# Performance work log

Measured on AMD Instinct MI355X. Metric: run time of the kernel, lower is better.

Reference implementation:

```python
import jax, jax.numpy as jnp
import numpy as np

MAX_SCALE_MUL = float(np.log(100.0))
EPS = 1e-12

def _l2norm(t):
    # F.normalize(dim=-1): x / max(||x||_2, eps)
    n = jnp.sqrt(jnp.sum(t * t, axis=-1, keepdims=True))
    return t / jnp.maximum(n, EPS)

def setup_inputs() -> dict:
    key = jax.random.key(0)
    ks = jax.random.split(key, 6)
    B, L, C, H = 2, 2048, 1024, 16
    x = jax.random.normal(ks[0], (B, L, C), dtype=jnp.float32)
    attn_bias = jax.random.normal(ks[1], (1, 1, L, L), dtype=jnp.float32) * 0.02
    W_qkv = jax.random.normal(ks[2], (3 * C, C), dtype=jnp.float32) * (1.0 / np.sqrt(C))
    q_bias = jnp.zeros((C,), dtype=jnp.float32)
    v_bias = jnp.zeros((C,), dtype=jnp.float32)
    scale_mul_1H11 = jnp.full((1, H, 1, 1), np.log(4.0), dtype=jnp.float32)
    W_proj = jax.random.normal(ks[3], (C, C), dtype=jnp.float32) * (1.0 / np.sqrt(C))
    b_proj = jnp.zeros((C,), dtype=jnp.float32)
    return {"x": x, "attn_bias": attn_bias, "W_qkv": W_qkv, "q_bias": q_bias,
            "v_bias": v_bias, "scale_mul_1H11": scale_mul_1H11,
            "W_proj": W_proj, "b_proj": b_proj}

def reference(x, attn_bias, W_qkv, q_bias, v_bias, scale_mul_1H11, W_proj, b_proj):
    B, L, C = x.shape
    H = scale_mul_1H11.shape[1]
    D = C // H
    # qkv projection (no linear bias) + concatenated (q_bias, 0, v_bias)
    bias = jnp.concatenate([q_bias, jnp.zeros_like(q_bias), v_bias])
    pre_qkv = jnp.einsum('blc,oc->blo', x, W_qkv) + bias  # (B,L,3C)
    qkv = pre_qkv.reshape(B, L, 3, H, D).transpose(2, 0, 3, 1, 4)  # (3,B,H,L,D)
    q, k, v = qkv[0], qkv[1], qkv[2]
    # cosine attention: l2-normalize q,k; q scaled by learned per-head scale
    scale_mul = jnp.exp(jnp.minimum(scale_mul_1H11, MAX_SCALE_MUL))
    q = _l2norm(q) * scale_mul
    k = _l2norm(k)
    # slow_attn_original with scale=1 (attn_l2_norm path)
    attn = jnp.einsum('bhld,bhmd->bhlm', q, k) + attn_bias  # (B,H,L,L)
    attn = jax.nn.softmax(attn, axis=-1)
    oup = jnp.einsum('bhlm,bhmd->bhld', attn, v)  # (B,H,L,D)
    oup = oup.transpose(0, 2, 1, 3).reshape(B, L, C)
    return jnp.einsum('blc,oc->blo', oup, W_proj) + b_proj
```

## Files before the change

### kernel.cpp

```cpp
#include <hip/hip_runtime.h>

typedef short bf16x8 __attribute__((ext_vector_type(8)));
typedef unsigned short u16x8 __attribute__((ext_vector_type(8)));
typedef float f32x4 __attribute__((ext_vector_type(4)));
typedef float f32x16 __attribute__((ext_vector_type(16)));
typedef unsigned int u32x2 __attribute__((ext_vector_type(2)));

#define LOG2E 1.44269504088896340736f

__device__ __forceinline__ float bf2f(unsigned short u) {
  union { unsigned int i; float f; } v; v.i = ((unsigned int)u) << 16; return v.f;
}
__device__ __forceinline__ unsigned short f2bf(float f) {
  union { float fl; unsigned int i; } v; v.fl = f;
  unsigned int r = v.i + 0x7FFFu + ((v.i >> 16) & 1u);
  return (unsigned short)(r >> 16);
}
__device__ __forceinline__ unsigned int cvt_pk_bf16(float lo, float hi) {
  unsigned int d;
  asm("v_cvt_pk_bf16_f32 %0, %1, %2" : "=v"(d) : "v"(lo), "v"(hi));
  return d;
}
__device__ __forceinline__ void perm_swap(unsigned int& a, unsigned int& b) {
  asm("v_permlane32_swap_b32 %0, %1" : "+v"(a), "+v"(b));
}
__device__ __forceinline__ bf16x8 mk8(unsigned int a, unsigned int b,
                                      unsigned int c, unsigned int d) {
  union { unsigned int u[4]; bf16x8 v; } r;
  r.u[0] = a; r.u[1] = b; r.u[2] = c; r.u[3] = d;
  return r.v;
}
__device__ __forceinline__ void gload_lds16(const void* g, void* l) {
  __builtin_amdgcn_global_load_lds(
      (const __attribute__((address_space(1))) void*)g,
      (__attribute__((address_space(3))) void*)l, 16, 0, 0);
}

__global__ __launch_bounds__(256) void cvt_all(const float* __restrict__ x,
                                               const float* __restrict__ wqkv,
                                               const float* __restrict__ wproj,
                                               unsigned short* __restrict__ xb,
                                               unsigned short* __restrict__ wqb,
                                               unsigned short* __restrict__ wpb) {
  int i = blockIdx.x * 256 + threadIdx.x;
  const float* src; unsigned short* dst; int off;
  if (i < 524288)       { src = x;     dst = xb;  off = i; }
  else if (i < 917504)  { src = wqkv;  dst = wqb; off = i - 524288; }
  else                  { src = wproj; dst = wpb; off = i - 917504; }
  float4 a = ((const float4*)src)[2 * off];
  float4 b = ((const float4*)src)[2 * off + 1];
  u16x8 o;
  o[0] = f2bf(a.x); o[1] = f2bf(a.y); o[2] = f2bf(a.z); o[3] = f2bf(a.w);
  o[4] = f2bf(b.x); o[5] = f2bf(b.y); o[6] = f2bf(b.z); o[7] = f2bf(b.w);
  ((u16x8*)dst)[off] = o;
}

__global__ __launch_bounds__(256) void prep_bias(const float* __restrict__ bias,
                                                 unsigned short* __restrict__ biasArr) {
  int tid = blockIdx.x * 256 + threadIdx.x;
  int kg = tid & 1;
  int l = (tid >> 1) & 63;
  int w = (tid >> 7) & 3;
  int kb = (tid >> 9) & 31;
  int qt = (tid >> 14) & 15;
  int q = qt * 128 + w * 32 + (l & 31);
  int kbase = kb * 64 + kg * 32 + (l >> 5) * 4;
  const float* src = bias + (size_t)q * 2048 + kbase;
  u16x8 oa, ob;
#pragma unroll
  for (int rr = 0; rr < 4; ++rr) {
    float4 g = *(const float4*)(src + rr * 8);
    unsigned short e0 = f2bf(g.x * LOG2E), e1 = f2bf(g.y * LOG2E);
    unsigned short e2 = f2bf(g.z * LOG2E), e3 = f2bf(g.w * LOG2E);
    if (rr < 2) {
      oa[rr * 4 + 0] = e0; oa[rr * 4 + 1] = e1; oa[rr * 4 + 2] = e2; oa[rr * 4 + 3] = e3;
    } else {
      ob[(rr - 2) * 4 + 0] = e0; ob[(rr - 2) * 4 + 1] = e1;
      ob[(rr - 2) * 4 + 2] = e2; ob[(rr - 2) * 4 + 3] = e3;
    }
  }
  int base = (((qt * 32 + kb) * 4 + w) * 4 + kg * 2) * 64 + l;
  ((u16x8*)biasArr)[base] = oa;
  ((u16x8*)biasArr)[base + 64] = ob;
}

template <bool F32OUT>
__global__ __launch_bounds__(256) void gemm_nt(const unsigned short* __restrict__ A,
                                               const unsigned short* __restrict__ B,
                                               void* __restrict__ Cout,
                                               const float* __restrict__ bias,
                                               int M, int N, int K) {
  __shared__ __align__(16) unsigned short a_lds[128 * 64];
  __shared__ __align__(16) unsigned short b_lds[128 * 64];
  const int t = threadIdx.x;
  const int lane = t & 63, w = t >> 6;
  const int wm = w >> 1, wn = w & 1;
  const int r16 = lane >> 4, c16 = lane & 15;
  const int m0 = blockIdx.y * 128, n0 = blockIdx.x * 128;
  f32x4 acc[4][4] = {};
  for (int k0 = 0; k0 < K; k0 += 64) {
#pragma unroll
    for (int i = 0; i < 4; ++i) {
      int s = i * 256 + t;
      int row = s >> 3, c = s & 7;
      int cs = c ^ (row & 7);
      gload_lds16(A + (size_t)(m0 + row) * K + k0 + cs * 8, (char*)a_lds + s * 16);
      gload_lds16(B + (size_t)(n0 + row) * K + k0 + cs * 8, (char*)b_lds + s * 16);
    }
    __syncthreads();
#pragma unroll
    for (int ks = 0; ks < 2; ++ks) {
      bf16x8 af[4], bfr[4];
#pragma unroll
      for (int mi = 0; mi < 4; ++mi) {
        int row = wm * 64 + mi * 16 + c16;
        int ch = (r16 + ks * 4) ^ (row & 7);
        af[mi] = *(const bf16x8*)&a_lds[row * 64 + ch * 8];
      }
#pragma unroll
      for (int ni = 0; ni < 4; ++ni) {
        int row = wn * 64 + ni * 16 + c16;
        int ch = (r16 + ks * 4) ^ (row & 7);
        bfr[ni] = *(const bf16x8*)&b_lds[row * 64 + ch * 8];
      }
#pragma unroll
      for (int mi = 0; mi < 4; ++mi)
#pragma unroll
        for (int ni = 0; ni < 4; ++ni)
          acc[mi][ni] = __builtin_amdgcn_mfma_f32_16x16x32_bf16(af[mi], bfr[ni], acc[mi][ni], 0, 0, 0);
    }
    __syncthreads();
  }
#pragma unroll
  for (int mi = 0; mi < 4; ++mi)
#pragma unroll
    for (int ni = 0; ni < 4; ++ni)
#pragma unroll
      for (int r = 0; r < 4; ++r) {
        int m = m0 + wm * 64 + mi * 16 + r16 * 4 + r;
        int n = n0 + wn * 64 + ni * 16 + c16;
        float v = acc[mi][ni][r];
        if constexpr (F32OUT) {
          ((float*)Cout)[(size_t)m * N + n] = v + bias[n];
        } else {
          ((unsigned short*)Cout)[(size_t)m * N + n] = f2bf(v);
        }
      }
}

template <bool F32OUT>
__global__ __launch_bounds__(256) void gemm_nt64(const unsigned short* __restrict__ A,
                                                 const unsigned short* __restrict__ B,
                                                 void* __restrict__ Cout,
                                                 const float* __restrict__ bias,
                                                 int M, int N, int K) {
  __shared__ __align__(16) unsigned short a_lds[128 * 64];
  __shared__ __align__(16) unsigned short b_lds[64 * 64];
  const int t = threadIdx.x;
  const int lane = t & 63, w = t >> 6;
  const int wm = w >> 1, wn = w & 1;
  const int r16 = lane >> 4, c16 = lane & 15;
  const int m0 = blockIdx.y * 128, n0 = blockIdx.x * 64;
  f32x4 acc[4][2] = {};
  for (int k0 = 0; k0 < K; k0 += 64) {
#pragma unroll
    for (int i = 0; i < 4; ++i) {
      int s = i * 256 + t;
      int row = s >> 3, c = s & 7;
      int cs = c ^ (row & 7);
      gload_lds16(A + (size_t)(m0 + row) * K + k0 + cs * 8, (char*)a_lds + s * 16);
    }
#pragma unroll
    for (int i = 0; i < 2; ++i) {
      int s = i * 256 + t;
      int row = s >> 3, c = s & 7;
      int cs = c ^ (row & 7);
      gload_lds16(B + (size_t)(n0 + row) * K + k0 + cs * 8, (char*)b_lds + s * 16);
    }
    __syncthreads();
#pragma unroll
    for (int ks = 0; ks < 2; ++ks) {
      bf16x8 af[4], bfr[2];
#pragma unroll
      for (int mi = 0; mi < 4; ++mi) {
        int row = wm * 64 + mi * 16 + c16;
        int ch = (r16 + ks * 4) ^ (row & 7);
        af[mi] = *(const bf16x8*)&a_lds[row * 64 + ch * 8];
      }
#pragma unroll
      for (int ni = 0; ni < 2; ++ni) {
        int row = wn * 32 + ni * 16 + c16;
        int ch = (r16 + ks * 4) ^ (row & 7);
        bfr[ni] = *(const bf16x8*)&b_lds[row * 64 + ch * 8];
      }
#pragma unroll
      for (int mi = 0; mi < 4; ++mi)
#pragma unroll
        for (int ni = 0; ni < 2; ++ni)
          acc[mi][ni] = __builtin_amdgcn_mfma_f32_16x16x32_bf16(af[mi], bfr[ni], acc[mi][ni], 0, 0, 0);
    }
    __syncthreads();
  }
#pragma unroll
  for (int mi = 0; mi < 4; ++mi)
#pragma unroll
    for (int ni = 0; ni < 2; ++ni)
#pragma unroll
      for (int r = 0; r < 4; ++r) {
        int m = m0 + wm * 64 + mi * 16 + r16 * 4 + r;
        int n = n0 + wn * 32 + ni * 16 + c16;
        float v = acc[mi][ni][r];
        if constexpr (F32OUT) {
          ((float*)Cout)[(size_t)m * N + n] = v + bias[n];
        } else {
          ((unsigned short*)Cout)[(size_t)m * N + n] = f2bf(v);
        }
      }
}

__global__ __launch_bounds__(256) void norm_pack(const unsigned short* __restrict__ pre,
                                                 const float* __restrict__ q_bias,
                                                 const float* __restrict__ v_bias,
                                                 const float* __restrict__ scale_mul,
                                                 unsigned short* __restrict__ qo,
                                                 unsigned short* __restrict__ ko,
                                                 unsigned short* __restrict__ vto) {
  __shared__ float tl[64][65];
  const int t = threadIdx.x;
  const int li = t >> 2, dq = t & 3;
  const int tile = blockIdx.x;
  const int sl = blockIdx.y;
  const int qkv = sl >> 4, h = sl & 15;
  const int b = tile >> 5, lt = tile & 31;
  const int l = lt * 64 + li;
  const int dbase = dq * 16;
  const unsigned short* src = pre + ((size_t)b * 2048 + l) * 3072 + qkv * 1024 + h * 64 + dbase;
  float v[16];
  bf16x8 x0 = *(const bf16x8*)src;
  bf16x8 x1 = *(const bf16x8*)(src + 8);
#pragma unroll
  for (int j = 0; j < 8; ++j) {
    v[j] = bf2f((unsigned short)x0[j]);
    v[8 + j] = bf2f((unsigned short)x1[j]);
  }
  if (qkv == 0) {
#pragma unroll
    for (int j = 0; j < 16; ++j) v[j] += q_bias[h * 64 + dbase + j];
  } else if (qkv == 2) {
#pragma unroll
    for (int j = 0; j < 16; ++j) v[j] += v_bias[h * 64 + dbase + j];
  }
  if (qkv < 2) {
    float ss = 0.f;
#pragma unroll
    for (int j = 0; j < 16; ++j) ss += v[j] * v[j];
    ss += __shfl_xor(ss, 1);
    ss += __shfl_xor(ss, 2);
    float inv = 1.0f / fmaxf(sqrtf(ss), 1e-12f);
    if (qkv == 0) inv *= __expf(fminf(scale_mul[h], 4.6051701859880914f));
    u16x8 o0, o1;
#pragma unroll
    for (int j = 0; j < 8; ++j) {
      o0[j] = f2bf(v[j] * inv);
      o1[j] = f2bf(v[8 + j] * inv);
    }
    unsigned short* dst = (qkv == 0 ? qo : ko) + ((size_t)(b * 16 + h) * 2048 + l) * 64 + dbase;
    *(u16x8*)dst = o0;
    *(u16x8*)(dst + 8) = o1;
  } else {
#pragma unroll
    for (int j = 0; j < 16; ++j) tl[li][dbase + j] = v[j];
    __syncthreads();
    const int d = li;
    const int lb = dq * 16;
    u16x8 o0, o1;
#pragma unroll
    for (int j = 0; j < 8; ++j) {
      o0[j] = f2bf(tl[lb + j][d]);
      o1[j] = f2bf(tl[lb + 8 + j][d]);
    }
    unsigned short* dst = vto + ((size_t)(b * 16 + h) * 64 + d) * 2048 + lt * 64 + lb;
    *(u16x8*)dst = o0;
    *(u16x8*)(dst + 8) = o1;
  }
}

__global__ __launch_bounds__(512, 4) void attn_fwd(const unsigned short* __restrict__ qb,
                                                   const unsigned short* __restrict__ kbuf,
                                                   const unsigned short* __restrict__ vtb,
                                                   const unsigned short* __restrict__ biasArr,
                                                   unsigned short* __restrict__ oup) {
  __shared__ __align__(16) unsigned short k_lds[2][4096];
  __shared__ __align__(16) unsigned short vt_lds[2][4096];
  __shared__ __align__(16) unsigned short b_lds[2][8192];
  const int t = threadIdx.x;
  const int lane = t & 63, w = t >> 6;
  const int sp = w >> 2;
  const int wq = w & 3;
  const int tt = t & 255;
  const int l31 = lane & 31, hi = lane >> 5;
  const int bid = blockIdx.x;
  const int swz = (bid & 7) * 64 + (bid >> 3);
  const int bh = swz >> 4;
  const int qt = swz & 15;
  const int q0 = qt * 128;
  const int h = bh & 15;
  const size_t base = (size_t)bh * 2048 * 64;
  const unsigned short* kp = kbuf + base + (size_t)(tt & 31) * 64 +
                             ((tt >> 6) & 3) * 16 + ((tt >> 5) & 1) * 8;
  const unsigned short* vp = vtb + base + (size_t)(tt & 31) * 2048 +
                             ((tt >> 6) & 3) * 16 + ((tt >> 5) & 1) * 8;
  const unsigned short* bsrc = biasArr + (size_t)qt * 262144 + tt * 8;
  bf16x8 qf[4];
  {
    const unsigned short* qp = qb + base + (size_t)(q0 + wq * 32 + l31) * 64 + hi * 8;
    qf[0] = *(const bf16x8*)qp;
    qf[1] = *(const bf16x8*)(qp + 16);
    qf[2] = *(const bf16x8*)(qp + 32);
    qf[3] = *(const bf16x8*)(qp + 48);
  }
  f32x16 o0 = {}, o1 = {};
  float ls = 0.f;

  for (int kbl = 0; kbl < 16; ++kbl) {
    const int kb = sp * 16 + kbl;
    gload_lds16(kp + (size_t)kb * 4096, (char*)k_lds[sp] + tt * 16);
    gload_lds16(kp + (size_t)kb * 4096 + 2048, (char*)k_lds[sp] + tt * 16 + 4096);
    gload_lds16(vp + kb * 64, (char*)vt_lds[sp] + tt * 16);
    gload_lds16(vp + kb * 64 + 32 * 2048, (char*)vt_lds[sp] + tt * 16 + 4096);
#pragma unroll
    for (int i = 0; i < 4; ++i)
      gload_lds16(bsrc + kb * 8192 + i * 2048, (char*)b_lds[sp] + tt * 16 + i * 4096);
    __syncthreads();
    const unsigned short* bl = b_lds[sp] + wq * 2048 + lane * 8;
#pragma unroll
    for (int kg = 0; kg < 2; ++kg) {
      f32x16 s = {};
      __builtin_amdgcn_s_setprio(1);
#pragma unroll
      for (int dc = 0; dc < 4; ++dc) {
        bf16x8 kf = *(const bf16x8*)&k_lds[sp][(kg * 4 + dc) * 512 + lane * 8];
        s = __builtin_amdgcn_mfma_f32_32x32x16_bf16(kf, qf[dc], s, 0, 0, 0);
      }
      __builtin_amdgcn_s_setprio(0);
      bf16x8 b0 = *(const bf16x8*)(bl + kg * 1024);
      bf16x8 b1 = *(const bf16x8*)(bl + kg * 1024 + 512);
      float p[16];
#pragma unroll
      for (int r = 0; r < 8; ++r) {
        p[r] = __builtin_amdgcn_exp2f(__builtin_fmaf(s[r], LOG2E, bf2f((unsigned short)b0[r])));
        p[8 + r] = __builtin_amdgcn_exp2f(__builtin_fmaf(s[8 + r], LOG2E, bf2f((unsigned short)b1[r])));
      }
#pragma unroll
      for (int r = 0; r < 16; ++r) ls += p[r];
      unsigned int x0 = cvt_pk_bf16(p[0], p[1]), x1 = cvt_pk_bf16(p[2], p[3]);
      unsigned int y0 = cvt_pk_bf16(p[4], p[5]), y1 = cvt_pk_bf16(p[6], p[7]);
      unsigned int z0 = cvt_pk_bf16(p[8], p[9]), z1 = cvt_pk_bf16(p[10], p[11]);
      unsigned int w0 = cvt_pk_bf16(p[12], p[13]), w1 = cvt_pk_bf16(p[14], p[15]);
      perm_swap(x0, y0); perm_swap(x1, y1); perm_swap(z0, w0); perm_swap(z1, w1);
      bf16x8 pfa = mk8(x0, x1, y0, y1);
      bf16x8 pfb = mk8(z0, z1, w0, w1);
      __builtin_amdgcn_s_setprio(1);
#pragma unroll
      for (int kc = 0; kc < 2; ++kc) {
        bf16x8 pfx = kc ? pfb : pfa;
        bf16x8 vf0 = *(const bf16x8*)&vt_lds[sp][(kg * 2 + kc) * 512 + lane * 8];
        bf16x8 vf1 = *(const bf16x8*)&vt_lds[sp][(4 + kg * 2 + kc) * 512 + lane * 8];
        o0 = __builtin_amdgcn_mfma_f32_32x32x16_bf16(vf0, pfx, o0, 0, 0, 0);
        o1 = __builtin_amdgcn_mfma_f32_32x32x16_bf16(vf1, pfx, o1, 0, 0, 0);
      }
      __builtin_amdgcn_s_setprio(0);
    }
    __syncthreads();
  }
  float* fO = (float*)b_lds;
  float* fL = (float*)k_lds;
  const int slot = wq * 64 + lane;
  if (sp == 1) {
#pragma unroll
    for (int i = 0; i < 16; ++i) {
      fO[i * 256 + slot] = o0[i];
      fO[(16 + i) * 256 + slot] = o1[i];
    }
    fL[slot] = ls;
  }
  __syncthreads();
  if (sp == 0) {
#pragma unroll
    for (int i = 0; i < 16; ++i) {
      o0[i] += fO[i * 256 + slot];
      o1[i] += fO[(16 + i) * 256 + slot];
    }
    ls += fL[slot];
    float lsum = ls + __shfl_xor(ls, 32);
    float inv = 1.0f / lsum;
    const int b = bh >> 4;
    unsigned short* orow = oup + ((size_t)b * 2048 + q0 + wq * 32 + l31) * 1024 + h * 64;
#pragma unroll
    for (int dg = 0; dg < 2; ++dg) {
#pragma unroll
      for (int rr = 0; rr < 4; ++rr) {
        float v0 = (dg ? o1[rr * 4 + 0] : o0[rr * 4 + 0]) * inv;
        float v1 = (dg ? o1[rr * 4 + 1] : o0[rr * 4 + 1]) * inv;
        float v2 = (dg ? o1[rr * 4 + 2] : o0[rr * 4 + 2]) * inv;
        float v3 = (dg ? o1[rr * 4 + 3] : o0[rr * 4 + 3]) * inv;
        u32x2 pk2;
        pk2[0] = cvt_pk_bf16(v0, v1);
        pk2[1] = cvt_pk_bf16(v2, v3);
        int d = dg * 32 + rr * 8 + hi * 4;
        *(u32x2*)(orow + d) = pk2;
      }
    }
  }
}

extern "C" void kernel_launch(void* const* d_in, const int* in_sizes, int n_in,
                              void* d_out, int out_size, void* d_ws, size_t ws_size,
                              hipStream_t stream) {
  const float* x = (const float*)d_in[0];
  const float* attn_bias = (const float*)d_in[1];
  const float* W_qkv = (const float*)d_in[2];
  const float* q_bias = (const float*)d_in[3];
  const float* v_bias = (const float*)d_in[4];
  const float* scale_mul = (const float*)d_in[5];
  const float* W_proj = (const float*)d_in[6];
  const float* b_proj = (const float*)d_in[7];
  float* out = (float*)d_out;
  char* ws = (char*)d_ws;

  unsigned short* x_bf = (unsigned short*)(ws + 0);
  unsigned short* wqkv_bf = (unsigned short*)(ws + 8388608);
  unsigned short* wproj_bf = (unsigned short*)(ws + 14680064);
  unsigned short* biasArr = (unsigned short*)(ws + 16777216);
  unsigned short* q_pk = (unsigned short*)(ws + 25165824);
  unsigned short* k_pk = (unsigned short*)(ws + 33554432);
  unsigned short* vt_pk = (unsigned short*)(ws + 41943040);
  unsigned short* oup_bf = (unsigned short*)(ws + 50331648);
  unsigned short* pre_qkv = (unsigned short*)(ws + 58720256);

  cvt_all<<<4096, 256, 0, stream>>>(x, W_qkv, W_proj, x_bf, wqkv_bf, wproj_bf);
  prep_bias<<<1024, 256, 0, stream>>>(attn_bias, biasArr);
  gemm_nt<false><<<dim3(24, 32), 256, 0, stream>>>(x_bf, wqkv_bf, (void*)pre_qkv, nullptr,
                                                   4096, 3072, 1024);
  norm_pack<<<dim3(64, 48), 256, 0, stream>>>(pre_qkv, q_bias, v_bias, scale_mul,
                                              q_pk, k_pk, vt_pk);
  attn_fwd<<<512, 512, 0, stream>>>(q_pk, k_pk, vt_pk, biasArr, oup_bf);
  gemm_nt64<true><<<dim3(16, 32), 256, 0, stream>>>(oup_bf, wproj_bf, (void*)out, b_proj,
                                                    4096, 1024, 1024);
}
```

Baseline: 135.4 us.

## Fuse QKV normalization and packing into GEMM epilogue; merge conversion kernels

Folds the bias add, L2 normalization, scale multiply and the Q/K/V-transpose packing into the epilogue of the QKV GEMM, so the intermediate pre_qkv buffer is no longer written and read back by a separate kernel. The fp32-to-bf16 conversion and the attention-bias preprocessing are merged into one launch. The epilogue now does 16-lane shuffle reductions and writes scattered 2-byte elements for Q/K and 8-byte transposed stores for V, which may coalesce worse than the old packing kernel.

```diff
diff --git a/kernel.cpp b/kernel.cpp
--- a/kernel.cpp
+++ b/kernel.cpp
@@ -2,6 +2,7 @@
 
 typedef short bf16x8 __attribute__((ext_vector_type(8)));
 typedef unsigned short u16x8 __attribute__((ext_vector_type(8)));
+typedef unsigned short u16x4 __attribute__((ext_vector_type(4)));
 typedef float f32x4 __attribute__((ext_vector_type(4)));
 typedef float f32x16 __attribute__((ext_vector_type(16)));
 typedef unsigned int u32x2 __attribute__((ext_vector_type(2)));
@@ -36,60 +37,63 @@
       (__attribute__((address_space(3))) void*)l, 16, 0, 0);
 }
 
-__global__ __launch_bounds__(256) void cvt_all(const float* __restrict__ x,
-                                               const float* __restrict__ wqkv,
-                                               const float* __restrict__ wproj,
-                                               unsigned short* __restrict__ xb,
-                                               unsigned short* __restrict__ wqb,
-                                               unsigned short* __restrict__ wpb) {
+__global__ __launch_bounds__(256) void cvt_prep(const float* __restrict__ x,
+                                                const float* __restrict__ wqkv,
+                                                const float* __restrict__ wproj,
+                                                const float* __restrict__ bias,
+                                                unsigned short* __restrict__ xb,
+                                                unsigned short* __restrict__ wqb,
+                                                unsigned short* __restrict__ wpb,
+                                                unsigned short* __restrict__ biasArr) {
   int i = blockIdx.x * 256 + threadIdx.x;
-  const float* src; unsigned short* dst; int off;
-  if (i < 524288)       { src = x;     dst = xb;  off = i; }
-  else if (i < 917504)  { src = wqkv;  dst = wqb; off = i - 524288; }
-  else                  { src = wproj; dst = wpb; off = i - 917504; }
-  float4 a = ((const float4*)src)[2 * off];
-  float4 b = ((const float4*)src)[2 * off + 1];
-  u16x8 o;
-  o[0] = f2bf(a.x); o[1] = f2bf(a.y); o[2] = f2bf(a.z); o[3] = f2bf(a.w);
-  o[4] = f2bf(b.x); o[5] = f2bf(b.y); o[6] = f2bf(b.z); o[7] = f2bf(b.w);
-  ((u16x8*)dst)[off] = o;
-}
-
-__global__ __launch_bounds__(256) void prep_bias(const float* __restrict__ bias,
-                                                 unsigned short* __restrict__ biasArr) {
-  int tid = blockIdx.x * 256 + threadIdx.x;
-  int kg = tid & 1;
-  int l = (tid >> 1) & 63;
-  int w = (tid >> 7) & 3;
-  int kb = (tid >> 9) & 31;
-  int qt = (tid >> 14) & 15;
-  int q = qt * 128 + w * 32 + (l & 31);
-  int kbase = kb * 64 + kg * 32 + (l >> 5) * 4;
-  const float* src = bias + (size_t)q * 2048 + kbase;
-  u16x8 oa, ob;
-#pragma unroll
-  for (int rr = 0; rr < 4; ++rr) {
-    float4 g = *(const float4*)(src + rr * 8);
-    unsigned short e0 = f2bf(g.x * LOG2E), e1 = f2bf(g.y * LOG2E);
-    unsigned short e2 = f2bf(g.z * LOG2E), e3 = f2bf(g.w * LOG2E);
-    if (rr < 2) {
-      oa[rr * 4 + 0] = e0; oa[rr * 4 + 1] = e1; oa[rr * 4 + 2] = e2; oa[rr * 4 + 3] = e3;
-    } else {
-      ob[(rr - 2) * 4 + 0] = e0; ob[(rr - 2) * 4 + 1] = e1;
-      ob[(rr - 2) * 4 + 2] = e2; ob[(rr - 2) * 4 + 3] = e3;
-    }
-  }
-  int base = (((qt * 32 + kb) * 4 + w) * 4 + kg * 2) * 64 + l;
-  ((u16x8*)biasArr)[base] = oa;
-  ((u16x8*)biasArr)[base + 64] = ob;
-}
-
-template <bool F32OUT>
-__global__ __launch_bounds__(256) void gemm_nt(const unsigned short* __restrict__ A,
-                                               const unsigned short* __restrict__ B,
-                                               void* __restrict__ Cout,
-                                               const float* __restrict__ bias,
-                                               int M, int N, int K) {
+  if (i < 1048576) {
+    const float* src; unsigned short* dst; int off;
+    if (i < 524288)       { src = x;     dst = xb;  off = i; }
+    else if (i < 917504)  { src = wqkv;  dst = wqb; off = i - 524288; }
+    else                  { src = wproj; dst = wpb; off = i - 917504; }
+    float4 a = ((const float4*)src)[2 * off];
+    float4 b = ((const float4*)src)[2 * off + 1];
+    u16x8 o;
+    o[0] = f2bf(a.x); o[1] = f2bf(a.y); o[2] = f2bf(a.z); o[3] = f2bf(a.w);
+    o[4] = f2bf(b.x); o[5] = f2bf(b.y); o[6] = f2bf(b.z); o[7] = f2bf(b.w);
+    ((u16x8*)dst)[off] = o;
+  } else {
+    int tid = i - 1048576;
+    int kg = tid & 1;
+    int l = (tid >> 1) & 63;
+    int w = (tid >> 7) & 3;
+    int kb = (tid >> 9) & 31;
+    int qt = (tid >> 14) & 15;
+    int q = qt * 128 + w * 32 + (l & 31);
+    int kbase = kb * 64 + kg * 32 + (l >> 5) * 4;
+    const float* src = bias + (size_t)q * 2048 + kbase;
+    u16x8 oa, ob;
+#pragma unroll
+    for (int rr = 0; rr < 4; ++rr) {
+      float4 g = *(const float4*)(src + rr * 8);
+      unsigned short e0 = f2bf(g.x * LOG2E), e1 = f2bf(g.y * LOG2E);
+      unsigned short e2 = f2bf(g.z * LOG2E), e3 = f2bf(g.w * LOG2E);
+      if (rr < 2) {
+        oa[rr * 4 + 0] = e0; oa[rr * 4 + 1] = e1; oa[rr * 4 + 2] = e2; oa[rr * 4 + 3] = e3;
+      } else {
+        ob[(rr - 2) * 4 + 0] = e0; ob[(rr - 2) * 4 + 1] = e1;
+        ob[(rr - 2) * 4 + 2] = e2; ob[(rr - 2) * 4 + 3] = e3;
+      }
+    }
+    int base = (((qt * 32 + kb) * 4 + w) * 4 + kg * 2) * 64 + l;
+    ((u16x8*)biasArr)[base] = oa;
+    ((u16x8*)biasArr)[base + 64] = ob;
+  }
+}
+
+__global__ __launch_bounds__(256) void gemm_qkv(const unsigned short* __restrict__ A,
+                                                const unsigned short* __restrict__ B,
+                                                const float* __restrict__ q_bias,
+                                                const float* __restrict__ v_bias,
+                                                const float* __restrict__ scale_mul,
+                                                unsigned short* __restrict__ qo,
+                                                unsigned short* __restrict__ ko,
+                                                unsigned short* __restrict__ vto) {
   __shared__ __align__(16) unsigned short a_lds[128 * 64];
   __shared__ __align__(16) unsigned short b_lds[128 * 64];
   const int t = threadIdx.x;
@@ -98,14 +102,14 @@
   const int r16 = lane >> 4, c16 = lane & 15;
   const int m0 = blockIdx.y * 128, n0 = blockIdx.x * 128;
   f32x4 acc[4][4] = {};
-  for (int k0 = 0; k0 < K; k0 += 64) {
+  for (int k0 = 0; k0 < 1024; k0 += 64) {
 #pragma unroll
     for (int i = 0; i < 4; ++i) {
       int s = i * 256 + t;
       int row = s >> 3, c = s & 7;
       int cs = c ^ (row & 7);
-      gload_lds16(A + (size_t)(m0 + row) * K + k0 + cs * 8, (char*)a_lds + s * 16);
-      gload_lds16(B + (size_t)(n0 + row) * K + k0 + cs * 8, (char*)b_lds + s * 16);
+      gload_lds16(A + (size_t)(m0 + row) * 1024 + k0 + cs * 8, (char*)a_lds + s * 16);
+      gload_lds16(B + (size_t)(n0 + row) * 1024 + k0 + cs * 8, (char*)b_lds + s * 16);
     }
     __syncthreads();
 #pragma unroll
@@ -131,21 +135,57 @@
     }
     __syncthreads();
   }
-#pragma unroll
-  for (int mi = 0; mi < 4; ++mi)
-#pragma unroll
-    for (int ni = 0; ni < 4; ++ni)
+  const int tp = n0 >> 10;
+  const int nq = n0 & 1023;
+  const int h = (nq >> 6) + wn;
+  const int bb = (m0 >= 2048) ? 1 : 0;
+  const int l0 = (m0 & 2047) + wm * 64;
+  if (tp == 2) {
+    float bias_d[4];
+#pragma unroll
+    for (int ni = 0; ni < 4; ++ni) bias_d[ni] = v_bias[h * 64 + ni * 16 + c16];
+    unsigned short* dstb = vto + (size_t)(bb * 16 + h) * 64 * 2048;
+#pragma unroll
+    for (int mi = 0; mi < 4; ++mi)
+#pragma unroll
+      for (int ni = 0; ni < 4; ++ni) {
+        int d = ni * 16 + c16;
+        u16x4 ov;
+#pragma unroll
+        for (int r = 0; r < 4; ++r) ov[r] = f2bf(acc[mi][ni][r] + bias_d[ni]);
+        *(u16x4*)(dstb + (size_t)d * 2048 + l0 + mi * 16 + r16 * 4) = ov;
+      }
+  } else {
+    float bias_d[4] = {0.f, 0.f, 0.f, 0.f};
+    float qscale = 1.0f;
+    if (tp == 0) {
+#pragma unroll
+      for (int ni = 0; ni < 4; ++ni) bias_d[ni] = q_bias[h * 64 + ni * 16 + c16];
+      qscale = __expf(fminf(scale_mul[h], 4.6051701859880914f));
+    }
+    unsigned short* dst = (tp == 0 ? qo : ko) + (size_t)(bb * 16 + h) * 2048 * 64;
+#pragma unroll
+    for (int mi = 0; mi < 4; ++mi)
 #pragma unroll
       for (int r = 0; r < 4; ++r) {
-        int m = m0 + wm * 64 + mi * 16 + r16 * 4 + r;
-        int n = n0 + wn * 64 + ni * 16 + c16;
-        float v = acc[mi][ni][r];
-        if constexpr (F32OUT) {
-          ((float*)Cout)[(size_t)m * N + n] = v + bias[n];
-        } else {
-          ((unsigned short*)Cout)[(size_t)m * N + n] = f2bf(v);
+        float vv[4];
+        float ss = 0.f;
+#pragma unroll
+        for (int ni = 0; ni < 4; ++ni) {
+          vv[ni] = acc[mi][ni][r] + bias_d[ni];
+          ss += vv[ni] * vv[ni];
         }
-      }
+        ss += __shfl_xor(ss, 1);
+        ss += __shfl_xor(ss, 2);
+        ss += __shfl_xor(ss, 4);
+        ss += __shfl_xor(ss, 8);
+        float inv = qscale / fmaxf(sqrtf(ss), 1e-12f);
+        int l = l0 + mi * 16 + r16 * 4 + r;
+#pragma unroll
+        for (int ni = 0; ni < 4; ++ni)
+          dst[(size_t)l * 64 + ni * 16 + c16] = f2bf(vv[ni] * inv);
+      }
+  }
 }
 
 template <bool F32OUT>
@@ -216,73 +256,6 @@
           ((unsigned short*)Cout)[(size_t)m * N + n] = f2bf(v);
         }
       }
-}
-
-__global__ __launch_bounds__(256) void norm_pack(const unsigned short* __restrict__ pre,
-                                                 const float* __restrict__ q_bias,
-                                                 const float* __restrict__ v_bias,
-                                                 const float* __restrict__ scale_mul,
-                                                 unsigned short* __restrict__ qo,
-                                                 unsigned short* __restrict__ ko,
-                                                 unsigned short* __restrict__ vto) {
-  __shared__ float tl[64][65];
-  const int t = threadIdx.x;
-  const int li = t >> 2, dq = t & 3;
-  const int tile = blockIdx.x;
-  const int sl = blockIdx.y;
-  const int qkv = sl >> 4, h = sl & 15;
-  const int b = tile >> 5, lt = tile & 31;
-  const int l = lt * 64 + li;
-  const int dbase = dq * 16;
-  const unsigned short* src = pre + ((size_t)b * 2048 + l) * 3072 + qkv * 1024 + h * 64 + dbase;
-  float v[16];
-  bf16x8 x0 = *(const bf16x8*)src;
-  bf16x8 x1 = *(const bf16x8*)(src + 8);
-#pragma unroll
-  for (int j = 0; j < 8; ++j) {
-    v[j] = bf2f((unsigned short)x0[j]);
-    v[8 + j] = bf2f((unsigned short)x1[j]);
-  }
-  if (qkv == 0) {
-#pragma unroll
-    for (int j = 0; j < 16; ++j) v[j] += q_bias[h * 64 + dbase + j];
-  } else if (qkv == 2) {
-#pragma unroll
-    for (int j = 0; j < 16; ++j) v[j] += v_bias[h * 64 + dbase + j];
-  }
-  if (qkv < 2) {
-    float ss = 0.f;
-#pragma unroll
-    for (int j = 0; j < 16; ++j) ss += v[j] * v[j];
-    ss += __shfl_xor(ss, 1);
-    ss += __shfl_xor(ss, 2);
-    float inv = 1.0f / fmaxf(sqrtf(ss), 1e-12f);
-    if (qkv == 0) inv *= __expf(fminf(scale_mul[h], 4.6051701859880914f));
-    u16x8 o0, o1;
-#pragma unroll
-    for (int j = 0; j < 8; ++j) {
-      o0[j] = f2bf(v[j] * inv);
-      o1[j] = f2bf(v[8 + j] * inv);
-    }
-    unsigned short* dst = (qkv == 0 ? qo : ko) + ((size_t)(b * 16 + h) * 2048 + l) * 64 + dbase;
-    *(u16x8*)dst = o0;
-    *(u16x8*)(dst + 8) = o1;
-  } else {
-#pragma unroll
-    for (int j = 0; j < 16; ++j) tl[li][dbase + j] = v[j];
-    __syncthreads();
-    const int d = li;
-    const int lb = dq * 16;
-    u16x8 o0, o1;
-#pragma unroll
-    for (int j = 0; j < 8; ++j) {
-      o0[j] = f2bf(tl[lb + j][d]);
-      o1[j] = f2bf(tl[lb + 8 + j][d]);
-    }
-    unsigned short* dst = vto + ((size_t)(b * 16 + h) * 64 + d) * 2048 + lt * 64 + lb;
-    *(u16x8*)dst = o0;
-    *(u16x8*)(dst + 8) = o1;
-  }
 }
 
 __global__ __launch_bounds__(512, 4) void attn_fwd(const unsigned short* __restrict__ qb,
@@ -436,14 +409,11 @@
   unsigned short* k_pk = (unsigned short*)(ws + 33554432);
   unsigned short* vt_pk = (unsigned short*)(ws + 41943040);
   unsigned short* oup_bf = (unsigned short*)(ws + 50331648);
-  unsigned short* pre_qkv = (unsigned short*)(ws + 58720256);
-
-  cvt_all<<<4096, 256, 0, stream>>>(x, W_qkv, W_proj, x_bf, wqkv_bf, wproj_bf);
-  prep_bias<<<1024, 256, 0, stream>>>(attn_bias, biasArr);
-  gemm_nt<false><<<dim3(24, 32), 256, 0, stream>>>(x_bf, wqkv_bf, (void*)pre_qkv, nullptr,
-                                                   4096, 3072, 1024);
-  norm_pack<<<dim3(64, 48), 256, 0, stream>>>(pre_qkv, q_bias, v_bias, scale_mul,
-                                              q_pk, k_pk, vt_pk);
+
+  cvt_prep<<<5120, 256, 0, stream>>>(x, W_qkv, W_proj, attn_bias,
+                                     x_bf, wqkv_bf, wproj_bf, biasArr);
+  gemm_qkv<<<dim3(24, 32), 256, 0, stream>>>(x_bf, wqkv_bf, q_bias, v_bias, scale_mul,
+                                             q_pk, k_pk, vt_pk);
   attn_fwd<<<512, 512, 0, stream>>>(q_pk, k_pk, vt_pk, biasArr, oup_bf);
   gemm_nt64<true><<<dim3(16, 32), 256, 0, stream>>>(oup_bf, wproj_bf, (void*)out, b_proj,
                                                     4096, 1024, 1024);
```

Result: no change. 133.7 us (-1.2%).
